# Kernel optimization log

Measured on AMD Instinct MI355X. Metric: run time of the kernel, lower is better.

## Reference

```python
import jax, jax.numpy as jnp
import numpy as np

IN_SIZE = 4096
OUT_SIZE = 4096
RANK = 64
LEG = 16  # 4096 ** (1/3)
BATCH = 16384


def setup_inputs() -> dict:
    key = jax.random.key(0)
    k_x, k1, k2, k3, kb = jax.random.split(key, 5)
    bound = 1.0 / np.sqrt(IN_SIZE)
    u = lambda k, shape: jax.random.uniform(k, shape, jnp.float32, -bound, bound)
    return {
        "x": jax.random.normal(k_x, (BATCH, IN_SIZE), dtype=jnp.float32),
        "first_core": u(k1, (LEG, RANK, LEG)),
        "middle_core": u(k2, (LEG, RANK, RANK, LEG)),
        "last_core": u(k3, (LEG, RANK, LEG)),
        "bias": u(kb, (OUT_SIZE,)),
    }


def reference(x, first_core, middle_core, last_core, bias):
    # x: [B, 4096] -> [B, 16, 16, 16]
    xr = x.reshape(-1, LEG, LEG, LEG)
    # Faithful to original: j and b are summed independently (not shared).
    # res: [in1, out1, in2, rank, out2]
    res = jnp.einsum('ijk,abcd->ikacd', first_core, middle_core)
    # addlastcore: A has 5 dims 'abcde'; output 'abc' + 'e' + 'ik' -> 'abceik'
    # res: [in1, out1, in2, out2, in3, out3]
    res = jnp.einsum('abcde,ijk->abceik', res, last_core)
    # contract input legs with x: [B, out1, out2, out3]
    out = jnp.einsum('iabc,axbycz->ixyz', xr, res)
    return out.reshape(-1, OUT_SIZE) + bias
```

## Files before the change

kernel.cpp:

```cpp
#include <hip/hip_runtime.h>


#define LEG 16

__global__ __launch_bounds__(256) void mpo_prep(
    const float* __restrict__ first, const float* __restrict__ middle,
    const float* __restrict__ last, float* __restrict__ W)
{
    __shared__ float red[256];
    const int t = threadIdx.x;
    const int blk = blockIdx.x;
    if (blk == 0) {
        const int xo = t >> 4, a = t & 15;
        float s = 0.f;
        #pragma unroll 8
        for (int j = 0; j < 64; ++j) s += first[a * 1024 + j * 16 + xo];
        W[t] = s;
    } else if (blk == 1) {
        const int z = t >> 4, c = t & 15;
        float s = 0.f;
        #pragma unroll 8
        for (int j = 0; j < 64; ++j) s += last[c * 1024 + j * 16 + z];
        W[512 + t] = s;
    } else {
        const int b = blk - 2;
        const int g = t >> 4, y = t & 15;
        float s = 0.f;
        for (int r1 = g; r1 < 64; r1 += 16) {
            const float* p = middle + (size_t)b * 65536 + (size_t)r1 * 1024 + y;
            #pragma unroll 8
            for (int r2 = 0; r2 < 64; ++r2) s += p[r2 * 16];
        }
        red[t] = s;
        __syncthreads();
        if (t < 16) {
            float tot = 0.f;
            #pragma unroll
            for (int g2 = 0; g2 < 16; ++g2) tot += red[g2 * 16 + t];
            W[256 + t * 16 + b] = tot;
        }
    }
}

__global__ __launch_bounds__(256, 4) void mpo_main(
    const float* __restrict__ x, const float* __restrict__ W,
    const float* __restrict__ bias, float* __restrict__ out)
{
    __shared__ float bufA[4352];
    __shared__ float bufB[4224];

    const int t = threadIdx.x;
    const size_t row = blockIdx.x;
    const float* xrow = x + row * 4096;
    float* orow = out + row * 4096;

    float4 bv[4];
    #pragma unroll
    for (int i = 0; i < 4; ++i)
        bv[i] = *(const float4*)(bias + t * 16 + i * 4);

    #pragma unroll
    for (int i = 0; i < 4; ++i) {
        float4 v = *(const float4*)(xrow + (i * 256 + t) * 4);
        *(float4*)(bufA + (i * 256 + t) * 4) = v;
    }
    __syncthreads();

    const float* WF = W;
    const float* WM = W + 256;
    const float* WL = W + 512;

    {
        float xa[16];
        #pragma unroll
        for (int a = 0; a < 16; ++a) xa[a] = bufA[a * 256 + t];
        #pragma unroll
        for (int q = 0; q < 4; ++q) {
            float acc[4] = {0.f, 0.f, 0.f, 0.f};
            #pragma unroll
            for (int a = 0; a < 16; ++a) {
                #pragma unroll
                for (int j = 0; j < 4; ++j)
                    acc[j] += xa[a] * WF[(q * 4 + j) * 16 + a];
            }
            #pragma unroll
            for (int j = 0; j < 4; ++j)
                bufB[(q * 4 + j) * 264 + t] = acc[j];
        }
    }
    __syncthreads();

    {
        const int x_ = t >> 4, c_ = t & 15;
        float tb[16];
        #pragma unroll
        for (int b = 0; b < 16; ++b) tb[b] = bufB[x_ * 264 + b * 16 + c_];
        #pragma unroll
        for (int q = 0; q < 4; ++q) {
            float acc[4] = {0.f, 0.f, 0.f, 0.f};
            #pragma unroll
            for (int b = 0; b < 16; ++b) {
                #pragma unroll
                for (int j = 0; j < 4; ++j)
                    acc[j] += tb[b] * WM[(q * 4 + j) * 16 + b];
            }
            #pragma unroll
            for (int j = 0; j < 4; ++j)
                bufA[(x_ * 16 + q * 4 + j) * 17 + c_] = acc[j];
        }
    }
    __syncthreads();

    {
        float tc[16];
        #pragma unroll
        for (int c = 0; c < 16; ++c) tc[c] = bufA[t * 17 + c];
        #pragma unroll
        for (int q = 0; q < 4; ++q) {
            float acc[4] = {bv[q].x, bv[q].y, bv[q].z, bv[q].w};
            #pragma unroll
            for (int c = 0; c < 16; ++c) {
                #pragma unroll
                for (int j = 0; j < 4; ++j)
                    acc[j] += tc[c] * WL[(q * 4 + j) * 16 + c];
            }
            float4 o;
            o.x = acc[0]; o.y = acc[1]; o.z = acc[2]; o.w = acc[3];
            *(float4*)(orow + t * 16 + q * 4) = o;
        }
    }
}

extern "C" void kernel_launch(void* const* d_in, const int* in_sizes, int n_in,
                              void* d_out, int out_size, void* d_ws, size_t ws_size,
                              hipStream_t stream) {
    const float* x      = (const float*)d_in[0];
    const float* first  = (const float*)d_in[1];
    const float* middle = (const float*)d_in[2];
    const float* last   = (const float*)d_in[3];
    const float* bias   = (const float*)d_in[4];
    float* out = (float*)d_out;
    float* W   = (float*)d_ws;

    const int Brows = in_sizes[0] / 4096;

    hipLaunchKernelGGL(mpo_prep, dim3(18), dim3(256), 0, stream,
                       first, middle, last, W);
    hipLaunchKernelGGL(mpo_main, dim3(Brows), dim3(256), 0, stream,
                       x, W, bias, out);
}
```

Measured before the change: 152.3 us.

## Use persistent grid with register prefetch of next row and nontemporal loads/stores

The main kernel now launches a fixed grid of up to 1024 blocks that loop over rows with a grid stride. Each block prefetches the next row of x into registers while computing the current one, overlapping global loads with the three small contractions. Loads and stores use nontemporal builtins to avoid polluting caches with streamed data. This adds an extra barrier per row and holds 16 more registers per thread, which may reduce occupancy.

```diff
diff --git a/kernel.cpp b/kernel.cpp
--- a/kernel.cpp
+++ b/kernel.cpp
@@ -2,6 +2,8 @@
 
 
 #define LEG 16
+
+typedef float f4 __attribute__((ext_vector_type(4)));
 
 __global__ __launch_bounds__(256) void mpo_prep(
     const float* __restrict__ first, const float* __restrict__ middle,
@@ -44,89 +46,107 @@
 
 __global__ __launch_bounds__(256, 4) void mpo_main(
     const float* __restrict__ x, const float* __restrict__ W,
-    const float* __restrict__ bias, float* __restrict__ out)
+    const float* __restrict__ bias, float* __restrict__ out, int nrows)
 {
     __shared__ float bufA[4352];
     __shared__ float bufB[4224];
 
     const int t = threadIdx.x;
-    const size_t row = blockIdx.x;
-    const float* xrow = x + row * 4096;
-    float* orow = out + row * 4096;
 
-    float4 bv[4];
+    f4 bv[4];
     #pragma unroll
     for (int i = 0; i < 4; ++i)
-        bv[i] = *(const float4*)(bias + t * 16 + i * 4);
-
-    #pragma unroll
-    for (int i = 0; i < 4; ++i) {
-        float4 v = *(const float4*)(xrow + (i * 256 + t) * 4);
-        *(float4*)(bufA + (i * 256 + t) * 4) = v;
-    }
-    __syncthreads();
+        bv[i] = *(const f4*)(bias + t * 16 + i * 4);
 
     const float* WF = W;
     const float* WM = W + 256;
     const float* WL = W + 512;
 
+    f4 xr[4];
     {
-        float xa[16];
+        const float* xrow = x + (size_t)blockIdx.x * 4096;
         #pragma unroll
-        for (int a = 0; a < 16; ++a) xa[a] = bufA[a * 256 + t];
+        for (int i = 0; i < 4; ++i)
+            xr[i] = __builtin_nontemporal_load((const f4*)(xrow + (i * 256 + t) * 4));
+    }
+
+    for (int row = blockIdx.x; row < nrows; row += gridDim.x) {
         #pragma unroll
-        for (int q = 0; q < 4; ++q) {
-            float acc[4] = {0.f, 0.f, 0.f, 0.f};
+        for (int i = 0; i < 4; ++i)
+            *(f4*)(bufA + (i * 256 + t) * 4) = xr[i];
+        __syncthreads();
+
+        {
+            const int nrow = row + (int)gridDim.x;
+            if (nrow < nrows) {
+                const float* nx = x + (size_t)nrow * 4096;
+                #pragma unroll
+                for (int i = 0; i < 4; ++i)
+                    xr[i] = __builtin_nontemporal_load((const f4*)(nx + (i * 256 + t) * 4));
+            }
+        }
+
+        {
+            float xa[16];
             #pragma unroll
-            for (int a = 0; a < 16; ++a) {
+            for (int a = 0; a < 16; ++a) xa[a] = bufA[a * 256 + t];
+            #pragma unroll
+            for (int q = 0; q < 4; ++q) {
+                float acc[4] = {0.f, 0.f, 0.f, 0.f};
+                #pragma unroll
+                for (int a = 0; a < 16; ++a) {
+                    #pragma unroll
+                    for (int j = 0; j < 4; ++j)
+                        acc[j] += xa[a] * WF[(q * 4 + j) * 16 + a];
+                }
                 #pragma unroll
                 for (int j = 0; j < 4; ++j)
-                    acc[j] += xa[a] * WF[(q * 4 + j) * 16 + a];
+                    bufB[(q * 4 + j) * 264 + t] = acc[j];
             }
+        }
+        __syncthreads();
+
+        {
+            const int x_ = t >> 4, c_ = t & 15;
+            float tb[16];
             #pragma unroll
-            for (int j = 0; j < 4; ++j)
-                bufB[(q * 4 + j) * 264 + t] = acc[j];
-        }
-    }
-    __syncthreads();
-
-    {
-        const int x_ = t >> 4, c_ = t & 15;
-        float tb[16];
-        #pragma unroll
-        for (int b = 0; b < 16; ++b) tb[b] = bufB[x_ * 264 + b * 16 + c_];
-        #pragma unroll
-        for (int q = 0; q < 4; ++q) {
-            float acc[4] = {0.f, 0.f, 0.f, 0.f};
+            for (int b = 0; b < 16; ++b) tb[b] = bufB[x_ * 264 + b * 16 + c_];
             #pragma unroll
-            for (int b = 0; b < 16; ++b) {
+            for (int q = 0; q < 4; ++q) {
+                float acc[4] = {0.f, 0.f, 0.f, 0.f};
+                #pragma unroll
+                for (int b = 0; b < 16; ++b) {
+                    #pragma unroll
+                    for (int j = 0; j < 4; ++j)
+                        acc[j] += tb[b] * WM[(q * 4 + j) * 16 + b];
+                }
                 #pragma unroll
                 for (int j = 0; j < 4; ++j)
-                    acc[j] += tb[b] * WM[(q * 4 + j) * 16 + b];
+                    bufA[(x_ * 16 + q * 4 + j) * 17 + c_] = acc[j];
             }
-            #pragma unroll
-            for (int j = 0; j < 4; ++j)
-                bufA[(x_ * 16 + q * 4 + j) * 17 + c_] = acc[j];
         }
-    }
-    __syncthreads();
+        __syncthreads();
 
-    {
         float tc[16];
         #pragma unroll
         for (int c = 0; c < 16; ++c) tc[c] = bufA[t * 17 + c];
-        #pragma unroll
-        for (int q = 0; q < 4; ++q) {
-            float acc[4] = {bv[q].x, bv[q].y, bv[q].z, bv[q].w};
+        __syncthreads();
+
+        {
+            float* orow = out + (size_t)row * 4096;
             #pragma unroll
-            for (int c = 0; c < 16; ++c) {
+            for (int q = 0; q < 4; ++q) {
+                float acc[4] = {bv[q].x, bv[q].y, bv[q].z, bv[q].w};
                 #pragma unroll
-                for (int j = 0; j < 4; ++j)
-                    acc[j] += tc[c] * WL[(q * 4 + j) * 16 + c];
+                for (int c = 0; c < 16; ++c) {
+                    #pragma unroll
+                    for (int j = 0; j < 4; ++j)
+                        acc[j] += tc[c] * WL[(q * 4 + j) * 16 + c];
+                }
+                f4 o;
+                o.x = acc[0]; o.y = acc[1]; o.z = acc[2]; o.w = acc[3];
+                __builtin_nontemporal_store(o, (f4*)(orow + t * 16 + q * 4));
             }
-            float4 o;
-            o.x = acc[0]; o.y = acc[1]; o.z = acc[2]; o.w = acc[3];
-            *(float4*)(orow + t * 16 + q * 4) = o;
         }
     }
 }
@@ -143,9 +163,11 @@
     float* W   = (float*)d_ws;
 
     const int Brows = in_sizes[0] / 4096;
+    int grid = 1024;
+    if (grid > Brows) grid = Brows;
 
     hipLaunchKernelGGL(mpo_prep, dim3(18), dim3(256), 0, stream,
                        first, middle, last, W);
-    hipLaunchKernelGGL(mpo_main, dim3(Brows), dim3(256), 0, stream,
-                       x, W, bias, out);
+    hipLaunchKernelGGL(mpo_main, dim3(grid), dim3(256), 0, stream,
+                       x, W, bias, out, Brows);
 }
```

After: 458.2 us. +200.9%, slower.
